# Kernel tuning notes

Measured on AMD Instinct MI355X. Metric: run time of the kernel, lower is better.

Reference implementation:

```python
import jax, jax.numpy as jnp
import numpy as np

B, C, H, W = 16, 256, 32, 32
AD, SC, R = 16, 32, 4


def _conv1x1(x, w, b):
    # x: [B,Cin,H,W], w: [Cout,Cin], b: [Cout]
    return jnp.einsum('oc,bchw->bohw', w, x) + b[None, :, None, None]


def setup_inputs() -> dict:
    key = jax.random.key(0)
    ks = jax.random.split(key, 12)
    p = lambda k, shape: (jax.random.normal(k, shape, dtype=jnp.float32) * 0.02)
    return {
        'x': jax.random.normal(ks[0], (B, C, H, W), dtype=jnp.float32),
        'fc1_w': p(ks[1], (C // R, C)), 'fc1_b': jnp.zeros((C // R,), jnp.float32),
        'fc2_w': p(ks[2], (C, C // R)), 'fc2_b': jnp.zeros((C,), jnp.float32),
        'qkv_w': p(ks[3], (AD * 2 + SC, SC)), 'qkv_b': jnp.zeros((AD * 2 + SC,), jnp.float32),
        'proj_w': p(ks[4], (SC, SC)), 'proj_b': jnp.zeros((SC,), jnp.float32),
        'ffn1_w': p(ks[5], (4 * C, C)), 'ffn1_b': jnp.zeros((4 * C,), jnp.float32),
        'ffn2_w': p(ks[6], (C, 4 * C)), 'ffn2_b': jnp.zeros((C,), jnp.float32),
    }


def reference(x, fc1_w, fc1_b, fc2_w, fc2_b, qkv_w, qkv_b, proj_w, proj_b,
              ffn1_w, ffn1_b, ffn2_w, ffn2_b):
    # --- DynamicChannelSelect: SE gate then channel split ---
    s = x.mean(axis=(2, 3), keepdims=True)                       # [B,C,1,1]
    s = jax.nn.relu(_conv1x1(s, fc1_w, fc1_b))
    s = jax.nn.sigmoid(_conv1x1(s, fc2_w, fc2_b))
    xg = x * s
    attn_part, non_attn_part = xg[:, :SC], xg[:, SC:]

    # --- SHSA: single-head self-attention on SC channels ---
    qkv = _conv1x1(attn_part, qkv_w, qkv_b)                      # [B,2*AD+SC,H,W]
    q = qkv[:, :AD].reshape(B, AD, H * W)
    k = qkv[:, AD:2 * AD].reshape(B, AD, H * W)
    v = qkv[:, 2 * AD:].reshape(B, SC, H * W)
    scale = AD ** -0.5
    attn = jax.nn.softmax(jnp.einsum('bcn,bcm->bnm', q, k) * scale, axis=-1)  # [B,N,N]
    out = jnp.einsum('bcm,bnm->bcn', v, attn).reshape(B, SC, H, W)
    attn_out = _conv1x1(out, proj_w, proj_b)

    # --- concat + 1x1-conv FFN ---
    y = jnp.concatenate([attn_out, non_attn_part], axis=1)       # [B,C,H,W]
    h = jax.nn.relu(_conv1x1(y, ffn1_w, ffn1_b))                 # [B,4C,H,W]
    return _conv1x1(h, ffn2_w, ffn2_b)                           # [B,C,H,W]
```

## Files before the change

kernel.cpp:

```cpp
#include <hip/hip_runtime.h>
#include <cstdint>
#include <cstddef>

#define BB 16
#define CC 256
#define NP 1024

typedef __attribute__((ext_vector_type(8))) short bf16x8;
typedef __attribute__((ext_vector_type(4))) float f32x4;
typedef unsigned short u16;

__device__ __forceinline__ u16 f2bf(float f) {
    union { float f; uint32_t u; } v; v.f = f;
    uint32_t u = v.u;
    return (u16)((u + 0x7FFFu + ((u >> 16) & 1u)) >> 16);
}

__global__ __launch_bounds__(256)
void se_mean_conv_kernel(const float* __restrict__ x, float* __restrict__ s_mean,
                         const float* __restrict__ w1, u16* __restrict__ d1,
                         const float* __restrict__ w2, u16* __restrict__ d2) {
    int blk = blockIdx.x;
    int t = threadIdx.x;
    if (blk < BB * CC) {
        const float* p = x + (size_t)blk * NP;
        float4 v = *(const float4*)(p + t * 4);
        float s = (v.x + v.y) + (v.z + v.w);
#pragma unroll
        for (int off = 32; off; off >>= 1) s += __shfl_down(s, off, 64);
        __shared__ float red[4];
        if ((t & 63) == 0) red[t >> 6] = s;
        __syncthreads();
        if (t == 0) s_mean[blk] = (red[0] + red[1] + red[2] + red[3]) * (1.0f / NP);
    } else {
        int blk2 = blk - BB * CC;
        const float* src = (blk2 < 256) ? w1 : w2;
        u16* dst = (blk2 < 256) ? d1 : d2;
        int i = ((blk2 & 255) * 256 + t) * 4;
        float4 v = *(const float4*)(src + i);
        ushort4 o;
        o.x = f2bf(v.x); o.y = f2bf(v.y); o.z = f2bf(v.z); o.w = f2bf(v.w);
        *(ushort4*)(dst + i) = o;
    }
}

__global__ __launch_bounds__(256)
void se_mlp_kernel(const float* __restrict__ s_mean,
                   const float* __restrict__ fc1_w, const float* __restrict__ fc1_b,
                   const float* __restrict__ fc2_w, const float* __restrict__ fc2_b,
                   float* __restrict__ sig) {
    int b = blockIdx.x, t = threadIdx.x;
    __shared__ float sm[256];
    __shared__ float part[4][64];
    __shared__ float h1[64];
    sm[t] = s_mean[b * 256 + t];
    __syncthreads();
    int to = t & 63, g = t >> 6;
    float a = 0.f;
#pragma unroll 8
    for (int c = 0; c < 64; ++c) a += fc1_w[to * 256 + g * 64 + c] * sm[g * 64 + c];
    part[g][to] = a;
    __syncthreads();
    if (t < 64) h1[t] = fmaxf(part[0][t] + part[1][t] + part[2][t] + part[3][t] + fc1_b[t], 0.f);
    __syncthreads();
    float acc = fc2_b[t];
#pragma unroll 8
    for (int j = 0; j < 64; ++j) acc += fc2_w[t * 64 + j] * h1[j];
    sig[b * 256 + t] = 1.f / (1.f + __expf(-acc));
}

__global__ __launch_bounds__(256)
void scale_transpose_qkv_kernel(const float* __restrict__ x, const float* __restrict__ sig,
                                const float* __restrict__ qW, const float* __restrict__ qB,
                                u16* __restrict__ ygt, u16* __restrict__ Qt,
                                u16* __restrict__ Kt, u16* __restrict__ Vb) {
    int nt = blockIdx.x, ct = blockIdx.y, b = blockIdx.z;
    __shared__ float tile[64][65];
    __shared__ float ws[64 * 32];
    __shared__ float bs[64];
    __shared__ float vtile[32][64];
    __shared__ float sig_l[64];
    int t = threadIdx.x;
    const float* Xb = x + ((size_t)b * CC + ct * 64) * NP + nt * 64;
    if (t < 64) sig_l[t] = sig[b * 256 + ct * 64 + t];
    if (ct == 0) {
        for (int e = t; e < 2048; e += 256) ws[e] = qW[e];
        if (t < 64) bs[t] = qB[t];
    }
#pragma unroll
    for (int p = 0; p < 4; ++p) {
        int e = t + p * 256;
        int c = e >> 4, n4 = (e & 15) * 4;
        float4 v = *(const float4*)&Xb[(size_t)c * NP + n4];
        tile[c][n4] = v.x; tile[c][n4 + 1] = v.y; tile[c][n4 + 2] = v.z; tile[c][n4 + 3] = v.w;
    }
    __syncthreads();
    u16* Yb = ygt + ((size_t)b * NP + nt * 64) * CC + ct * 64;
#pragma unroll
    for (int p = 0; p < 4; ++p) {
        int e = t + p * 256;
        int n = e >> 4, c4 = (e & 15) * 4;
        if (ct * 64 + c4 >= 32) {
            ushort4 o;
            o.x = f2bf(tile[c4][n] * sig_l[c4]);
            o.y = f2bf(tile[c4 + 1][n] * sig_l[c4 + 1]);
            o.z = f2bf(tile[c4 + 2][n] * sig_l[c4 + 2]);
            o.w = f2bf(tile[c4 + 3][n] * sig_l[c4 + 3]);
            *(ushort4*)&Yb[(size_t)n * CC + c4] = o;
        }
    }
    if (ct == 0) {
        int nn = t & 63, g = t >> 6;
        int n = nt * 64 + nn;
        float xs[32];
#pragma unroll
        for (int c = 0; c < 32; ++c) xs[c] = tile[c][nn] * sig_l[c];
        float acc[16];
#pragma unroll
        for (int oc = 0; oc < 16; ++oc) {
            int o = g * 16 + oc;
            float a = bs[o];
#pragma unroll
            for (int c = 0; c < 32; ++c) a += ws[o * 32 + c] * xs[c];
            acc[oc] = a;
        }
        if (g == 0) {
            u16* qr = Qt + ((size_t)b * NP + n) * 32;
            ushort4 z4; z4.x = 0; z4.y = 0; z4.z = 0; z4.w = 0;
#pragma unroll
            for (int j = 0; j < 16; j += 4) {
                ushort4 o4;
                o4.x = f2bf(acc[j] * 0.25f);     o4.y = f2bf(acc[j + 1] * 0.25f);
                o4.z = f2bf(acc[j + 2] * 0.25f); o4.w = f2bf(acc[j + 3] * 0.25f);
                *(ushort4*)&qr[j] = o4;
            }
            *(ushort4*)&qr[16] = z4; *(ushort4*)&qr[20] = z4;
            *(ushort4*)&qr[24] = z4; *(ushort4*)&qr[28] = z4;
        } else if (g == 1) {
            u16* kr = Kt + ((size_t)b * NP + n) * 32;
            ushort4 z4; z4.x = 0; z4.y = 0; z4.z = 0; z4.w = 0;
#pragma unroll
            for (int j = 0; j < 16; j += 4) {
                ushort4 k4;
                k4.x = f2bf(acc[j]);     k4.y = f2bf(acc[j + 1]);
                k4.z = f2bf(acc[j + 2]); k4.w = f2bf(acc[j + 3]);
                *(ushort4*)&kr[j] = k4;
            }
            *(ushort4*)&kr[16] = z4; *(ushort4*)&kr[20] = z4;
            *(ushort4*)&kr[24] = z4; *(ushort4*)&kr[28] = z4;
        } else {
#pragma unroll
            for (int oc = 0; oc < 16; ++oc) vtile[(g - 2) * 16 + oc][nn] = acc[oc];
        }
        __syncthreads();
        for (int e = t; e < 2048; e += 256) {
            int c = e >> 6, nn2 = e & 63;
            Vb[(size_t)b * 32 * NP + (size_t)c * NP + nt * 64 + nn2] = f2bf(vtile[c][nn2]);
        }
    }
}

__global__ __launch_bounds__(256)
void attn_mfma_kernel(const u16* __restrict__ Qt, const u16* __restrict__ Kt,
                      const u16* __restrict__ Vb,
                      const float* __restrict__ proj_w, const float* __restrict__ proj_b,
                      u16* __restrict__ ygt) {
    int b = blockIdx.x & 15;
    int n0 = (blockIdx.x >> 4) * 16;
    __shared__ __align__(16) u16 P_lds[4][16][40];
    __shared__ float al_lds[4][16];
    __shared__ float sm_lds[4][16];
    __shared__ float sl_lds[4][16];
    __shared__ float O_lds[4][16][33];
    __shared__ float pw_s[32][32];
    __shared__ float pb_s[32];
    int t = threadIdx.x;
    int w = t >> 6, lane = t & 63;
    int q = lane >> 4, idx = lane & 15;

    for (int e = t; e < 1024; e += 256) pw_s[e >> 5][e & 31] = proj_w[e];
    if (t < 32) pb_s[t] = proj_b[t];
    __syncthreads();

    const u16* Qb = Qt + (size_t)b * NP * 32;
    const u16* Kb = Kt + (size_t)b * NP * 32;
    const u16* Vp = Vb + (size_t)b * 32 * NP;

    int nrow = n0 + idx;
    bf16x8 aq = *(const bf16x8*)&Qb[(size_t)nrow * 32 + q * 8];

    f32x4 O0 = {0.f, 0.f, 0.f, 0.f}, O1 = {0.f, 0.f, 0.f, 0.f};
    float m_run[4] = {-1e30f, -1e30f, -1e30f, -1e30f};
    float l_run[4] = {0.f, 0.f, 0.f, 0.f};

    int mbase = w * 256;
    for (int m0 = mbase; m0 < mbase + 256; m0 += 32) {
        bf16x8 bk0 = *(const bf16x8*)&Kb[(size_t)(m0 + idx) * 32 + q * 8];
        bf16x8 bk1 = *(const bf16x8*)&Kb[(size_t)(m0 + 16 + idx) * 32 + q * 8];
        bf16x8 va0 = *(const bf16x8*)&Vp[(size_t)idx * NP + m0 + q * 8];
        bf16x8 va1 = *(const bf16x8*)&Vp[(size_t)(16 + idx) * NP + m0 + q * 8];
        f32x4 z = {0.f, 0.f, 0.f, 0.f};
        f32x4 S0 = __builtin_amdgcn_mfma_f32_16x16x32_bf16(aq, bk0, z, 0, 0, 0);
        f32x4 S1 = __builtin_amdgcn_mfma_f32_16x16x32_bf16(aq, bk1, z, 0, 0, 0);
        float mx[4], p0[4], p1[4], alpha[4];
#pragma unroll
        for (int r = 0; r < 4; ++r) mx[r] = fmaxf(S0[r], S1[r]);
#pragma unroll
        for (int off = 1; off < 16; off <<= 1)
#pragma unroll
            for (int r = 0; r < 4; ++r) mx[r] = fmaxf(mx[r], __shfl_xor(mx[r], off, 64));
#pragma unroll
        for (int r = 0; r < 4; ++r) {
            float nm = fmaxf(m_run[r], mx[r]);
            alpha[r] = __expf(m_run[r] - nm);
            m_run[r] = nm;
            p0[r] = __expf(S0[r] - nm);
            p1[r] = __expf(S1[r] - nm);
        }
#pragma unroll
        for (int r = 0; r < 4; ++r) {
            float s = p0[r] + p1[r];
#pragma unroll
            for (int off = 1; off < 16; off <<= 1) s += __shfl_xor(s, off, 64);
            l_run[r] = l_run[r] * alpha[r] + s;
        }
#pragma unroll
        for (int r = 0; r < 4; ++r) {
            P_lds[w][q * 4 + r][idx]      = f2bf(p0[r]);
            P_lds[w][q * 4 + r][idx + 16] = f2bf(p1[r]);
        }
        if (idx == 0) {
#pragma unroll
            for (int r = 0; r < 4; ++r) al_lds[w][q * 4 + r] = alpha[r];
        }
        float an = al_lds[w][idx];
#pragma unroll
        for (int r = 0; r < 4; ++r) { O0[r] *= an; O1[r] *= an; }
        bf16x8 pf = *(const bf16x8*)&P_lds[w][idx][q * 8];
        O0 = __builtin_amdgcn_mfma_f32_16x16x32_bf16(va0, pf, O0, 0, 0, 0);
        O1 = __builtin_amdgcn_mfma_f32_16x16x32_bf16(va1, pf, O1, 0, 0, 0);
    }
    if (idx == 0) {
#pragma unroll
        for (int r = 0; r < 4; ++r) {
            sm_lds[w][q * 4 + r] = m_run[r];
            sl_lds[w][q * 4 + r] = l_run[r];
        }
    }
#pragma unroll
    for (int r = 0; r < 4; ++r) {
        O_lds[w][idx][q * 4 + r]      = O0[r];
        O_lds[w][idx][q * 4 + r + 16] = O1[r];
    }
    __syncthreads();
    if (w == 0) {
        float m0_ = sm_lds[0][idx], m1 = sm_lds[1][idx], m2 = sm_lds[2][idx], m3 = sm_lds[3][idx];
        float gm = fmaxf(fmaxf(m0_, m1), fmaxf(m2, m3));
        float e0 = __expf(m0_ - gm), e1 = __expf(m1 - gm);
        float e2 = __expf(m2 - gm), e3 = __expf(m3 - gm);
        float linv = 1.f / (sl_lds[0][idx] * e0 + sl_lds[1][idx] * e1 +
                            sl_lds[2][idx] * e2 + sl_lds[3][idx] * e3);
#pragma unroll
        for (int r = 0; r < 4; ++r) {
            int c0 = q * 4 + r;
            O_lds[0][idx][c0] = (O_lds[0][idx][c0] * e0 + O_lds[1][idx][c0] * e1 +
                                 O_lds[2][idx][c0] * e2 + O_lds[3][idx][c0] * e3) * linv;
            int c1 = c0 + 16;
            O_lds[0][idx][c1] = (O_lds[0][idx][c1] * e0 + O_lds[1][idx][c1] * e1 +
                                 O_lds[2][idx][c1] * e2 + O_lds[3][idx][c1] * e3) * linv;
        }
        float o0[4], o1[4];
#pragma unroll
        for (int r = 0; r < 4; ++r) { o0[r] = pb_s[q * 4 + r]; o1[r] = pb_s[q * 4 + r + 16]; }
#pragma unroll
        for (int c = 0; c < 32; ++c) {
            float xv = O_lds[0][idx][c];
#pragma unroll
            for (int r = 0; r < 4; ++r) {
                o0[r] += pw_s[q * 4 + r][c] * xv;
                o1[r] += pw_s[q * 4 + r + 16][c] * xv;
            }
        }
        u16* yrow = ygt + ((size_t)b * NP + n0 + idx) * CC;
        ushort4 w0, w1;
        w0.x = f2bf(o0[0]); w0.y = f2bf(o0[1]); w0.z = f2bf(o0[2]); w0.w = f2bf(o0[3]);
        w1.x = f2bf(o1[0]); w1.y = f2bf(o1[1]); w1.z = f2bf(o1[2]); w1.w = f2bf(o1[3]);
        *(ushort4*)&yrow[q * 4] = w0;
        *(ushort4*)&yrow[q * 4 + 16] = w1;
    }
}

__global__ __launch_bounds__(256)
void ffn_fused_kernel(const u16* __restrict__ w1b, const u16* __restrict__ w2b,
                      const u16* __restrict__ ygt,
                      const float* __restrict__ bias1, const float* __restrict__ bias2,
                      float* __restrict__ out) {
    __shared__ __align__(16) u16 Ys[4][32][64];
    __shared__ __align__(16) u16 Hs[2][32][64];
    __shared__ float Bs1[1024];
    int t = threadIdx.x;
    int w = t >> 6, lane = t & 63;
    int q = lane >> 4, idx = lane & 15;
    int srow = lane >> 3;
    int gch = (lane & 7) ^ srow;
    int n0 = blockIdx.x * 32;

#pragma unroll
    for (int p = 0; p < 4; ++p) {
        int kb = p;
        int nb = w * 8;
        __builtin_amdgcn_global_load_lds(
            (const __attribute__((address_space(1))) void*)(ygt + (size_t)(n0 + nb + srow) * CC + kb * 64 + gch * 8),
            (__attribute__((address_space(3))) void*)(&Ys[kb][nb][0]),
            16, 0, 0);
    }
    for (int e = t; e < 1024; e += 256) Bs1[e] = bias1[e];

    f32x4 oacc[4][2];
#pragma unroll
    for (int f = 0; f < 4; ++f)
#pragma unroll
        for (int j = 0; j < 2; ++j) { f32x4 z = {0.f, 0.f, 0.f, 0.f}; oacc[f][j] = z; }

    __syncthreads();

    bf16x8 af[8];
    {
        const u16* a1 = w1b + ((size_t)(w * 16 + idx)) * CC;
#pragma unroll
        for (int s = 0; s < 8; ++s) af[s] = *(const bf16x8*)(a1 + s * 32 + q * 8);
    }

    for (int ch = 0; ch < 16; ++ch) {
        bf16x8 af2[4][2];
        const u16* a2 = w2b + ((size_t)(w * 64 + idx)) * 1024 + ch * 64;
#pragma unroll
        for (int f = 0; f < 4; ++f)
#pragma unroll
            for (int s2 = 0; s2 < 2; ++s2)
                af2[f][s2] = *(const bf16x8*)(a2 + (size_t)f * 16 * 1024 + s2 * 32 + q * 8);

        f32x4 hacc[2];
#pragma unroll
        for (int j = 0; j < 2; ++j) { f32x4 z = {0.f, 0.f, 0.f, 0.f}; hacc[j] = z; }
#pragma unroll
        for (int s = 0; s < 8; ++s) {
            int kb = s >> 1, hh = s & 1;
#pragma unroll
            for (int j = 0; j < 2; ++j) {
                bf16x8 yb = *(const bf16x8*)&Ys[kb][j * 16 + idx][(((q + 4 * hh) ^ (idx & 7)) * 8)];
                hacc[j] = __builtin_amdgcn_mfma_f32_16x16x32_bf16(af[s], yb, hacc[j], 0, 0, 0);
            }
        }
        int mbase = ch * 64 + w * 16 + q * 4;
        float b0 = Bs1[mbase], b1v = Bs1[mbase + 1], b2v = Bs1[mbase + 2], b3v = Bs1[mbase + 3];
        int chk_hi = w * 2 + (q >> 1);
#pragma unroll
        for (int j = 0; j < 2; ++j) {
            int n = j * 16 + idx;
            int chk = chk_hi ^ (n & 7);
            uint32_t lo = (uint32_t)f2bf(fmaxf(hacc[j][0] + b0, 0.f)) |
                          ((uint32_t)f2bf(fmaxf(hacc[j][1] + b1v, 0.f)) << 16);
            uint32_t hi = (uint32_t)f2bf(fmaxf(hacc[j][2] + b2v, 0.f)) |
                          ((uint32_t)f2bf(fmaxf(hacc[j][3] + b3v, 0.f)) << 16);
            uint32_t* hp = (uint32_t*)&Hs[ch & 1][n][chk * 8 + (q & 1) * 4];
            hp[0] = lo; hp[1] = hi;
        }
        __syncthreads();
        if (ch + 1 < 16) {
            const u16* a1 = w1b + ((size_t)((ch + 1) * 64 + w * 16 + idx)) * CC;
#pragma unroll
            for (int s = 0; s < 8; ++s) af[s] = *(const bf16x8*)(a1 + s * 32 + q * 8);
        }
#pragma unroll
        for (int s2 = 0; s2 < 2; ++s2)
#pragma unroll
            for (int j = 0; j < 2; ++j) {
                bf16x8 hb = *(const bf16x8*)&Hs[ch & 1][j * 16 + idx][(((q + 4 * s2) ^ (idx & 7)) * 8)];
#pragma unroll
                for (int f = 0; f < 4; ++f)
                    oacc[f][j] = __builtin_amdgcn_mfma_f32_16x16x32_bf16(af2[f][s2], hb, oacc[f][j], 0, 0, 0);
            }
    }

    int b = n0 >> 10, nnb = n0 & 1023;
#pragma unroll
    for (int f = 0; f < 4; ++f) {
        int m2 = w * 64 + f * 16 + q * 4;
        float c0 = bias2[m2], c1 = bias2[m2 + 1], c2 = bias2[m2 + 2], c3 = bias2[m2 + 3];
#pragma unroll
        for (int j = 0; j < 2; ++j) {
            float* p = out + ((size_t)b * CC + m2) * NP + nnb + j * 16 + idx;
            f32x4 v = oacc[f][j];
            p[0]      = v.x + c0;
            p[NP]     = v.y + c1;
            p[2 * NP] = v.z + c2;
            p[3 * NP] = v.w + c3;
        }
    }
}

extern "C" void kernel_launch(void* const* d_in, const int* in_sizes, int n_in,
                              void* d_out, int out_size, void* d_ws, size_t ws_size,
                              hipStream_t stream) {
    const float* x      = (const float*)d_in[0];
    const float* fc1_w  = (const float*)d_in[1];
    const float* fc1_b  = (const float*)d_in[2];
    const float* fc2_w  = (const float*)d_in[3];
    const float* fc2_b  = (const float*)d_in[4];
    const float* qkv_w  = (const float*)d_in[5];
    const float* qkv_b  = (const float*)d_in[6];
    const float* proj_w = (const float*)d_in[7];
    const float* proj_b = (const float*)d_in[8];
    const float* ffn1_w = (const float*)d_in[9];
    const float* ffn1_b = (const float*)d_in[10];
    const float* ffn2_w = (const float*)d_in[11];
    const float* ffn2_b = (const float*)d_in[12];
    float* out = (float*)d_out;

    u16* w1b = (u16*)d_ws;
    u16* w2b = w1b + 262144;
    u16* ygt = w2b + 262144;
    u16* scratch = ygt + (size_t)BB * NP * CC;
    float* s_mean = (float*)scratch;
    float* sig    = s_mean + BB * CC;
    u16* Qt = (u16*)(sig + BB * CC);
    u16* Kt = Qt + (size_t)BB * NP * 32;
    u16* Vb = Kt + (size_t)BB * NP * 32;

    se_mean_conv_kernel<<<BB * CC + 512, 256, 0, stream>>>(x, s_mean, ffn1_w, w1b, ffn2_w, w2b);
    se_mlp_kernel<<<BB, 256, 0, stream>>>(s_mean, fc1_w, fc1_b, fc2_w, fc2_b, sig);
    scale_transpose_qkv_kernel<<<dim3(16, 4, BB), 256, 0, stream>>>(
        x, sig, qkv_w, qkv_b, ygt, Qt, Kt, Vb);
    attn_mfma_kernel<<<BB * 64, 256, 0, stream>>>(Qt, Kt, Vb, proj_w, proj_b, ygt);

    ffn_fused_kernel<<<512, 256, 0, stream>>>(w1b, w2b, ygt, ffn1_b, ffn2_b, out);
}
```

Before: 196.7 us.

## Restructure fused FFN kernel into 64-token tiles with LDS-staged W2 and split-K reduction

The fused FFN kernel now uses 512-thread blocks that each handle 64 tokens instead of 32, halving the number of blocks and doubling reuse of each weight fetch. W2 slices are staged into LDS asynchronously via global_load_lds, and the hidden dimension is split across two wave halves, whose partial outputs are summed through LDS at the end. Blocks start at a chunk offset rotated by block index to spread weight-read traffic, and the next W1 fragment is prefetched into registers. The cost is much higher LDS usage (about 100KB), larger register footprint, and an extra reduction pass, which may limit occupancy on the 256-block grid.

```diff
diff --git a/kernel.cpp b/kernel.cpp
--- a/kernel.cpp
+++ b/kernel.cpp
@@ -290,112 +290,153 @@
     }
 }
 
-__global__ __launch_bounds__(256)
+__global__ __launch_bounds__(512, 2)
 void ffn_fused_kernel(const u16* __restrict__ w1b, const u16* __restrict__ w2b,
                       const u16* __restrict__ ygt,
                       const float* __restrict__ bias1, const float* __restrict__ bias2,
                       float* __restrict__ out) {
-    __shared__ __align__(16) u16 Ys[4][32][64];
-    __shared__ __align__(16) u16 Hs[2][32][64];
+    __shared__ __align__(16) u16 Ys[4][64][64];
+    __shared__ __align__(16) u16 Hs[2][64][64];
+    __shared__ __align__(16) u16 W2s[2][256][64];
     __shared__ float Bs1[1024];
     int t = threadIdx.x;
     int w = t >> 6, lane = t & 63;
     int q = lane >> 4, idx = lane & 15;
     int srow = lane >> 3;
     int gch = (lane & 7) ^ srow;
-    int n0 = blockIdx.x * 32;
-
-#pragma unroll
-    for (int p = 0; p < 4; ++p) {
-        int kb = p;
-        int nb = w * 8;
+    int n0 = blockIdx.x * 64;
+    int rot = blockIdx.x & 7;
+    int hh = w >> 2, wm = w & 3;
+
+#define ISSUE_W2S(sc_)                                                                     \
+    {                                                                                      \
+        _Pragma("unroll")                                                                  \
+        for (int e = 0; e < 8; ++e) {                                                      \
+            int hh2 = e >> 2, rnd = e & 3;                                                 \
+            int rw = rnd * 64 + w * 8;                                                     \
+            __builtin_amdgcn_global_load_lds(                                              \
+                (const __attribute__((address_space(1))) void*)(w2b + (size_t)(rw + srow) * 1024 + (sc_) * 128 + hh2 * 64 + gch * 8), \
+                (__attribute__((address_space(3))) void*)(&W2s[hh2][rw][0]),               \
+                16, 0, 0);                                                                 \
+        }                                                                                  \
+    }
+
+#define LOAD_AF(dst, sc_)                                                                  \
+    {                                                                                      \
+        const u16* a1 = w1b + ((size_t)((sc_) * 128 + w * 16 + idx)) * CC;                 \
+        _Pragma("unroll")                                                                  \
+        for (int s = 0; s < 8; ++s) dst[s] = *(const bf16x8*)(a1 + s * 32 + q * 8);        \
+    }
+
+#pragma unroll
+    for (int e = 0; e < 4; ++e) {
         __builtin_amdgcn_global_load_lds(
-            (const __attribute__((address_space(1))) void*)(ygt + (size_t)(n0 + nb + srow) * CC + kb * 64 + gch * 8),
-            (__attribute__((address_space(3))) void*)(&Ys[kb][nb][0]),
+            (const __attribute__((address_space(1))) void*)(ygt + (size_t)(n0 + w * 8 + srow) * CC + e * 64 + gch * 8),
+            (__attribute__((address_space(3))) void*)(&Ys[e][w * 8][0]),
             16, 0, 0);
     }
-    for (int e = t; e < 1024; e += 256) Bs1[e] = bias1[e];
-
-    f32x4 oacc[4][2];
+    Bs1[t] = bias1[t];
+    Bs1[t + 512] = bias1[t + 512];
+
+    f32x4 oacc[4][4];
 #pragma unroll
     for (int f = 0; f < 4; ++f)
 #pragma unroll
-        for (int j = 0; j < 2; ++j) { f32x4 z = {0.f, 0.f, 0.f, 0.f}; oacc[f][j] = z; }
-
-    __syncthreads();
-
+        for (int j = 0; j < 4; ++j) { f32x4 z = {0.f, 0.f, 0.f, 0.f}; oacc[f][j] = z; }
+
+    ISSUE_W2S(rot)
     bf16x8 af[8];
-    {
-        const u16* a1 = w1b + ((size_t)(w * 16 + idx)) * CC;
-#pragma unroll
-        for (int s = 0; s < 8; ++s) af[s] = *(const bf16x8*)(a1 + s * 32 + q * 8);
-    }
-
-    for (int ch = 0; ch < 16; ++ch) {
-        bf16x8 af2[4][2];
-        const u16* a2 = w2b + ((size_t)(w * 64 + idx)) * 1024 + ch * 64;
-#pragma unroll
-        for (int f = 0; f < 4; ++f)
-#pragma unroll
-            for (int s2 = 0; s2 < 2; ++s2)
-                af2[f][s2] = *(const bf16x8*)(a2 + (size_t)f * 16 * 1024 + s2 * 32 + q * 8);
-
-        f32x4 hacc[2];
-#pragma unroll
-        for (int j = 0; j < 2; ++j) { f32x4 z = {0.f, 0.f, 0.f, 0.f}; hacc[j] = z; }
+    LOAD_AF(af, rot)
+    __syncthreads();
+
+    for (int it = 0; it < 8; ++it) {
+        int sc  = (it + rot) & 7;
+        int scn = (it + 1 + rot) & 7;
+        bf16x8 afn[8];
+        if (it + 1 < 8) LOAD_AF(afn, scn)
+
+        f32x4 hacc[4];
+#pragma unroll
+        for (int j = 0; j < 4; ++j) { f32x4 z = {0.f, 0.f, 0.f, 0.f}; hacc[j] = z; }
 #pragma unroll
         for (int s = 0; s < 8; ++s) {
-            int kb = s >> 1, hh = s & 1;
-#pragma unroll
-            for (int j = 0; j < 2; ++j) {
-                bf16x8 yb = *(const bf16x8*)&Ys[kb][j * 16 + idx][(((q + 4 * hh) ^ (idx & 7)) * 8)];
+            int kb = s >> 1, h2 = s & 1;
+#pragma unroll
+            for (int j = 0; j < 4; ++j) {
+                bf16x8 yb = *(const bf16x8*)&Ys[kb][j * 16 + idx][(((q + 4 * h2) ^ (idx & 7)) * 8)];
                 hacc[j] = __builtin_amdgcn_mfma_f32_16x16x32_bf16(af[s], yb, hacc[j], 0, 0, 0);
             }
         }
-        int mbase = ch * 64 + w * 16 + q * 4;
-        float b0 = Bs1[mbase], b1v = Bs1[mbase + 1], b2v = Bs1[mbase + 2], b3v = Bs1[mbase + 3];
-        int chk_hi = w * 2 + (q >> 1);
-#pragma unroll
-        for (int j = 0; j < 2; ++j) {
+
+        int mb = sc * 128 + w * 16 + q * 4;
+        float b0 = Bs1[mb], b1v = Bs1[mb + 1], b2v = Bs1[mb + 2], b3v = Bs1[mb + 3];
+        int chk_hi = wm * 2 + (q >> 1);
+#pragma unroll
+        for (int j = 0; j < 4; ++j) {
             int n = j * 16 + idx;
             int chk = chk_hi ^ (n & 7);
             uint32_t lo = (uint32_t)f2bf(fmaxf(hacc[j][0] + b0, 0.f)) |
                           ((uint32_t)f2bf(fmaxf(hacc[j][1] + b1v, 0.f)) << 16);
             uint32_t hi = (uint32_t)f2bf(fmaxf(hacc[j][2] + b2v, 0.f)) |
                           ((uint32_t)f2bf(fmaxf(hacc[j][3] + b3v, 0.f)) << 16);
-            uint32_t* hp = (uint32_t*)&Hs[ch & 1][n][chk * 8 + (q & 1) * 4];
+            uint32_t* hp = (uint32_t*)&Hs[hh][n][chk * 8 + (q & 1) * 4];
             hp[0] = lo; hp[1] = hi;
         }
         __syncthreads();
-        if (ch + 1 < 16) {
-            const u16* a1 = w1b + ((size_t)((ch + 1) * 64 + w * 16 + idx)) * CC;
-#pragma unroll
-            for (int s = 0; s < 8; ++s) af[s] = *(const bf16x8*)(a1 + s * 32 + q * 8);
-        }
-#pragma unroll
-        for (int s2 = 0; s2 < 2; ++s2)
-#pragma unroll
-            for (int j = 0; j < 2; ++j) {
-                bf16x8 hb = *(const bf16x8*)&Hs[ch & 1][j * 16 + idx][(((q + 4 * s2) ^ (idx & 7)) * 8)];
+
+#pragma unroll
+        for (int s2 = 0; s2 < 2; ++s2) {
+            bf16x8 a2f[4];
+#pragma unroll
+            for (int f = 0; f < 4; ++f)
+                a2f[f] = *(const bf16x8*)&W2s[hh][wm * 64 + f * 16 + idx][(((q + 4 * s2) ^ (idx & 7)) * 8)];
+#pragma unroll
+            for (int j = 0; j < 4; ++j) {
+                bf16x8 hb = *(const bf16x8*)&Hs[hh][j * 16 + idx][(((q + 4 * s2) ^ (idx & 7)) * 8)];
 #pragma unroll
                 for (int f = 0; f < 4; ++f)
-                    oacc[f][j] = __builtin_amdgcn_mfma_f32_16x16x32_bf16(af2[f][s2], hb, oacc[f][j], 0, 0, 0);
-            }
-    }
-
-    int b = n0 >> 10, nnb = n0 & 1023;
-#pragma unroll
-    for (int f = 0; f < 4; ++f) {
-        int m2 = w * 64 + f * 16 + q * 4;
-        float c0 = bias2[m2], c1 = bias2[m2 + 1], c2 = bias2[m2 + 2], c3 = bias2[m2 + 3];
-#pragma unroll
-        for (int j = 0; j < 2; ++j) {
-            float* p = out + ((size_t)b * CC + m2) * NP + nnb + j * 16 + idx;
-            f32x4 v = oacc[f][j];
-            p[0]      = v.x + c0;
-            p[NP]     = v.y + c1;
-            p[2 * NP] = v.z + c2;
-            p[3 * NP] = v.w + c3;
+                    oacc[f][j] = __builtin_amdgcn_mfma_f32_16x16x32_bf16(a2f[f], hb, oacc[f][j], 0, 0, 0);
+            }
+        }
+        __syncthreads();
+
+        if (it + 1 < 8) {
+            ISSUE_W2S(scn)
+#pragma unroll
+            for (int s = 0; s < 8; ++s) af[s] = afn[s];
+        }
+    }
+#undef ISSUE_W2S
+#undef LOAD_AF
+
+    float* R = (float*)&W2s[0][0][0];
+    if (w >= 4) {
+#pragma unroll
+        for (int f = 0; f < 4; ++f)
+#pragma unroll
+            for (int j = 0; j < 4; ++j)
+#pragma unroll
+                for (int r = 0; r < 4; ++r)
+                    R[(wm * 64 + f * 16 + q * 4 + r) * 64 + j * 16 + idx] = oacc[f][j][r];
+    }
+    __syncthreads();
+    if (w < 4) {
+        int b = n0 >> 10, nnb = n0 & 1023;
+#pragma unroll
+        for (int f = 0; f < 4; ++f) {
+            int m2 = wm * 64 + f * 16 + q * 4;
+            float c0 = bias2[m2], c1 = bias2[m2 + 1], c2 = bias2[m2 + 2], c3 = bias2[m2 + 3];
+#pragma unroll
+            for (int j = 0; j < 4; ++j) {
+                int col = j * 16 + idx;
+                const float* Rp = &R[m2 * 64 + col];
+                float* p = out + ((size_t)b * CC + m2) * NP + nnb + col;
+                f32x4 v = oacc[f][j];
+                p[0]      = v.x + c0 + Rp[0];
+                p[NP]     = v.y + c1 + Rp[64];
+                p[2 * NP] = v.z + c2 + Rp[128];
+                p[3 * NP] = v.w + c3 + Rp[192];
+            }
         }
     }
 }
@@ -434,5 +475,5 @@
         x, sig, qkv_w, qkv_b, ygt, Qt, Kt, Vb);
     attn_mfma_kernel<<<BB * 64, 256, 0, stream>>>(Qt, Kt, Vb, proj_w, proj_b, ygt);
 
-    ffn_fused_kernel<<<512, 256, 0, stream>>>(w1b, w2b, ygt, ffn1_b, ffn2_b, out);
-}
+    ffn_fused_kernel<<<256, 512, 0, stream>>>(w1b, w2b, ygt, ffn1_b, ffn2_b, out);
+}
```

After: 162.7 us. 1.21x faster.
